# Kernel optimization log

Hardware: AMD Instinct MI355X
Metric: run time of the kernel (lower is better)

Reference implementation:

```python
import jax, jax.numpy as jnp
import numpy as np

# static config (matches init_kwargs / input_specs)
K = 3          # kernel_size
S = 1          # strides
FILTERS = 64
H = 128
W = 128
CIN = 128
OUT1 = (H - K) // S + 1   # 126
OUT2 = (W - K) // S + 1   # 126
N = OUT1 * K              # J2.shape[0] = 378
M = OUT2 * K              # J1.shape[1] = 378
L = OUT1 * OUT2           # output_lenght = 15876


def _build_phi_indices():
    # Faithful replication of set_indices_phi: column index of each of the
    # K*K ones in row (filter, i) of the sparse kernel (same for every filter).
    idx = np.zeros((L, K * K), dtype=np.int32)
    count, shift = 1, 0
    for i in range(L):
        if i == count * OUT2:
            count += 1
            shift += K + (K - 1) * M
        elif shift:
            shift += K
        else:
            shift += 1
        p = 0
        for block in range(K):
            for j in range(K):
                idx[i, p] = block * M + shift - 1 + j
                p += 1
    return idx

PHI_IDX = _build_phi_indices()                                   # (L, K*K)
# J2 @ x @ J1 with one-hot shift matrices == strided row/col gathers
R_IDX = (np.arange(OUT1)[:, None] * S + np.arange(K)[None, :]).reshape(-1)  # (N,)
C_IDX = (np.arange(OUT2)[:, None] * S + np.arange(K)[None, :]).reshape(-1)  # (M,)


def setup_inputs() -> dict:
    key = jax.random.key(0)
    k1, k2 = jax.random.split(key)
    inputs = jax.random.normal(k1, (1, H, W, CIN), dtype=jnp.float32)
    Lambda_in = jax.random.normal(k2, (1, N * M), dtype=jnp.float32)
    return {"inputs": inputs, "Lambda_in": Lambda_in}


def reference(inputs, Lambda_in):
    B = inputs.shape[0]  # must be 1 (tf.matmul batch broadcast with filters)
    # matrix_pad is identity for padding='VALID'
    flat = inputs.reshape(B, H * W, CIN)
    # faithful raw reshape from the source (NOT a transpose)
    x = flat.reshape(B, CIN, H, H)
    # inputs_y = J2 @ x @ J1  -> strided gathers with one-hot shift matrices
    y = x[:, :, R_IDX][:, :, :, C_IDX]        # (B, CIN, N, M)
    y = y.reshape(B, N * M, CIN)               # faithful raw reshape
    # sparse kernel (ones at PHI_IDX) right-multiplied by diag(Lambda_in)
    w = Lambda_in[0][PHI_IDX]                  # (L, K*K)
    g = y[:, PHI_IDX, :]                       # (B, L, K*K, CIN)
    out = jnp.einsum('blkc,lk->blc', g, w)     # (B, L, CIN)
    # tf.matmul broadcasts kernel batch dim (filters) against B=1
    out = jnp.broadcast_to(out[0][None], (FILTERS, L, CIN))
    out = out.reshape(FILTERS, OUT1, OUT1, CIN)
    return jax.nn.relu(out)
```

## Files before the change

### kernel.cpp

```cpp
#include <hip/hip_runtime.h>


#define L_TOT 15876

__global__ __launch_bounds__(128) void spectral_base_kernel(
    const float* __restrict__ x, const float* __restrict__ lam,
    float* __restrict__ out)
{
    __shared__ float s[128];
    const int l = blockIdx.x;
    const int t = threadIdx.x;
    const int row = l / 126;
    const int col = l - row * 126;

    float acc = 0.0f;
#pragma unroll
    for (int b3 = 0; b3 < 3; ++b3) {
#pragma unroll
        for (int j = 0; j < 3; ++j) {
            const unsigned phi = (unsigned)((3 * row + b3) * 378 + 3 * col + j);
            const unsigned n   = phi * 128u + (unsigned)t;
            const unsigned c   = n / 142884u;
            const unsigned rem = n - c * 142884u;
            const unsigned r   = rem / 378u;
            const unsigned ss  = rem - r * 378u;
            const unsigned src = c * 16384u + (r / 3u + r % 3u) * 128u + (ss / 3u + ss % 3u);
            acc = fmaf(x[src], lam[phi], acc);
        }
    }
    s[t] = fmaxf(acc, 0.0f);
    __syncthreads();

    const float4* s4 = (const float4*)s;
    float4* out4 = (float4*)out;
    const size_t lbase = (size_t)l * 32;
#pragma unroll
    for (int i = 0; i < 16; ++i) {
        const int idx = i * 128 + t;
        const int f = idx >> 5;
        const int v = idx & 31;
        out4[(size_t)f * (L_TOT * 32) + lbase + v] = s4[v];
    }
}

extern "C" void kernel_launch(void* const* d_in, const int* in_sizes, int n_in,
                              void* d_out, int out_size, void* d_ws, size_t ws_size,
                              hipStream_t stream) {
    const float* x   = (const float*)d_in[0];
    const float* lam = (const float*)d_in[1];
    float* out = (float*)d_out;

    spectral_base_kernel<<<L_TOT, 128, 0, stream>>>(x, lam, out);
}
```

Measured before the change: 109.0 us.

## Split compute and 64-way broadcast into two kernels with nontemporal stores

The single kernel, which computed one output row and scattered it to all 64 filter planes, becomes two kernels. The first computes plane 0 once with two rows per block and no shared memory. The second reads chunks of plane 0 and streams them with nontemporal vector stores to the other 63 planes, staggering the starting plane across blocks. This aims to make the write-bound broadcast more contiguous and bandwidth-friendly, at the cost of a second launch and a re-read of plane 0.

After: 119.9 us. +10.0%, slower.

```diff
diff --git a/kernel.cpp b/kernel.cpp
--- a/kernel.cpp
+++ b/kernel.cpp
@@ -1,15 +1,19 @@
 #include <hip/hip_runtime.h>
 
 
-#define L_TOT 15876
+#define L_TOT    15876
+#define PLANE_F4 (L_TOT * 32)
+#define CHUNK_F4 1024
 
-__global__ __launch_bounds__(128) void spectral_base_kernel(
+typedef float f4 __attribute__((ext_vector_type(4)));
+
+__global__ __launch_bounds__(256) void spectral_compute(
     const float* __restrict__ x, const float* __restrict__ lam,
     float* __restrict__ out)
 {
-    __shared__ float s[128];
-    const int l = blockIdx.x;
     const int t = threadIdx.x;
+    const int l = blockIdx.x * 2 + (t >> 7);
+    const int q = t & 127;
     const int row = l / 126;
     const int col = l - row * 126;
 
@@ -19,7 +23,7 @@
 #pragma unroll
         for (int j = 0; j < 3; ++j) {
             const unsigned phi = (unsigned)((3 * row + b3) * 378 + 3 * col + j);
-            const unsigned n   = phi * 128u + (unsigned)t;
+            const unsigned n   = phi * 128u + (unsigned)q;
             const unsigned c   = n / 142884u;
             const unsigned rem = n - c * 142884u;
             const unsigned r   = rem / 378u;
@@ -28,18 +32,35 @@
             acc = fmaf(x[src], lam[phi], acc);
         }
     }
-    s[t] = fmaxf(acc, 0.0f);
-    __syncthreads();
+    out[(size_t)l * 128 + q] = fmaxf(acc, 0.0f);
+}
 
-    const float4* s4 = (const float4*)s;
-    float4* out4 = (float4*)out;
-    const size_t lbase = (size_t)l * 32;
+__global__ __launch_bounds__(256) void spectral_bcast(float* __restrict__ out)
+{
+    const int t = threadIdx.x;
+    const size_t cbase = (size_t)blockIdx.x * CHUNK_F4;
+    const f4* p0 = (const f4*)out;
+    f4* o4 = (f4*)out;
+
+    f4  v[4];
+    bool ok[4];
+    int idx[4];
 #pragma unroll
-    for (int i = 0; i < 16; ++i) {
-        const int idx = i * 128 + t;
-        const int f = idx >> 5;
-        const int v = idx & 31;
-        out4[(size_t)f * (L_TOT * 32) + lbase + v] = s4[v];
+    for (int k = 0; k < 4; ++k) {
+        idx[k] = t + k * 256;
+        ok[k]  = (cbase + (size_t)idx[k]) < (size_t)PLANE_F4;
+        v[k]   = ok[k] ? p0[cbase + idx[k]] : (f4){0.f, 0.f, 0.f, 0.f};
+    }
+
+    int ff = 1 + (int)(blockIdx.x % 63u);
+#pragma unroll 1
+    for (int j = 0; j < 63; ++j) {
+        f4* dst = o4 + (size_t)ff * PLANE_F4 + cbase;
+#pragma unroll
+        for (int k = 0; k < 4; ++k)
+            if (ok[k]) __builtin_nontemporal_store(v[k], &dst[idx[k]]);
+        ++ff;
+        if (ff == 64) ff = 1;
     }
 }
 
@@ -50,5 +71,7 @@
     const float* lam = (const float*)d_in[1];
     float* out = (float*)d_out;
 
-    spectral_base_kernel<<<L_TOT, 128, 0, stream>>>(x, lam, out);
+    spectral_compute<<<L_TOT / 2, 256, 0, stream>>>(x, lam, out);
+    const int nblocks = (PLANE_F4 + CHUNK_F4 - 1) / CHUNK_F4;
+    spectral_bcast<<<nblocks, 256, 0, stream>>>(out);
 }
```
